# Optimization experiments

Measured on AMD Instinct MI355X. Metric: run time of the kernel, lower is better.

## Reference

```python
import jax, jax.numpy as jnp
import numpy as np

MAX_ITER = 10
EPS = 1e-4


def setup_inputs() -> dict:
    key = jax.random.key(0)
    k1, k2, k3 = jax.random.split(key, 3)
    B, N, M = 64, 1024, 1024
    s = jax.random.uniform(k1, (B, N, M), dtype=jnp.float32)
    nrows = jax.random.randint(k2, (B,), 0, N, dtype=jnp.int64 if jax.config.read('jax_enable_x64') else jnp.int32)
    ncols = jax.random.randint(k3, (B,), 0, M, dtype=nrows.dtype)
    return {"s": s, "nrows": nrows, "ncols": ncols}


def _sinkhorn(s, nrows, ncols):
    # Faithful to torch Sinkhorn.forward with exp=False, dummy_row=False.
    # The torch code builds [B,N,N]/[B,M,M] block-of-ones matrices and matmuls;
    # mathematically this is a masked column-sum (even iters) / row-sum (odd iters)
    # over the valid nrows[b] x ncols[b] block, followed by division inside the
    # block and zeroing outside it.
    B, N, M = s.shape
    row_mask = jnp.arange(N)[None, :] < nrows[:, None]            # [B, N]
    col_mask = jnp.arange(M)[None, :] < ncols[:, None]            # [B, M]
    mask = row_mask[:, :, None] & col_mask[:, None, :]            # [B, N, M]

    out = s + EPS
    for i in range(MAX_ITER):
        if i % 2 == 0:
            # column sums over valid rows -> [B, 1, M]
            sm = jnp.sum(jnp.where(row_mask[:, :, None], out, 0.0), axis=1, keepdims=True)
        else:
            # row sums over valid cols -> [B, N, 1]
            sm = jnp.sum(jnp.where(col_mask[:, None, :], out, 0.0), axis=2, keepdims=True)
        sm = jnp.where(sm == 0, 1.0, sm)  # guard (only affects masked-out entries)
        out = jnp.where(mask, out / sm, 0.0)
    return out


def reference(s, nrows, ncols):
    return _sinkhorn(s, nrows, ncols)
```

## Files before the change

kernel.cpp:

```cpp
#include <hip/hip_runtime.h>
#include <hip/hip_fp16.h>

#define EPS 1e-4f
constexpr int N_DIM  = 1024;
constexpr int M_DIM  = 1024;
constexpr int BATCH  = 64;
constexpr int NB     = 1024;
constexpr int NXCD   = 8;
constexpr int SLOTS  = NB / NXCD;
constexpr int NPHASE = 5;
constexpr int WPAD   = 256;
constexpr int CH     = 16;
constexpr int Q8MIN  = 64;


typedef float v4f __attribute__((ext_vector_type(4)));
__device__ __forceinline__ float4 ntload4(const float* p) {
    v4f v = __builtin_nontemporal_load((const v4f*)p);
    return make_float4(v[0], v[1], v[2], v[3]);
}
__device__ __forceinline__ void ntstore4(float* p, float4 q) {
    v4f v = {q.x, q.y, q.z, q.w};
    __builtin_nontemporal_store(v, (v4f*)p);
}

__device__ __forceinline__ unsigned enc8(float v) {
    int u = (int)__float_as_uint(v) + 0x00040000 - 0x3C000000;
    int b = u >> 19;
    return (unsigned)min(max(b, 16), 127);
}
__device__ __forceinline__ float dec8(unsigned b) {
    return b ? __uint_as_float((b << 19) + 0x3C000000u) : 0.f;
}

__global__ void zero_cnt(unsigned int* cnt) {
    const int t = threadIdx.x;
    if (t < NPHASE * BATCH) cnt[t] = 0u;
}

__device__ __forceinline__ void bat_barrier(unsigned int* cnt, int idx,
                                            unsigned int nact) {
    __syncthreads();
    if (threadIdx.x == 0) {
        __threadfence();
        atomicAdd(&cnt[idx], 1u);
        while (__hip_atomic_load(&cnt[idx], __ATOMIC_ACQUIRE,
                                 __HIP_MEMORY_SCOPE_AGENT) < nact)
            __builtin_amdgcn_s_sleep(8);
    }
    __syncthreads();
    __threadfence();
}

__device__ __forceinline__ void tp_store(__half* tp, size_t idx, float4 v) {
    union { __half2 h2[2]; uint2 u; } pk;
    pk.h2[0] = __floats2half2_rn(v.x, v.y);
    pk.h2[1] = __floats2half2_rn(v.z, v.w);
    *(uint2*)(tp + idx) = pk.u;
}

__global__ __launch_bounds__(256, 4)
void sinkhorn_xcd(const float* __restrict__ s,
                  const int* __restrict__ nrows,
                  const int* __restrict__ ncols,
                  __half* __restrict__ h,
                  __half* __restrict__ tp0,
                  __half* __restrict__ tp1,
                  unsigned int* __restrict__ cnt,
                  float* __restrict__ out)
{
    const int tid = threadIdx.x, lane = tid & 63, wv = tid >> 6;
    __shared__ int sR[BATCH];
    __shared__ int sBx[BATCH];
    __shared__ int sNb[BATCH];
    __shared__ int sSt[BATCH];

    if (tid < BATCH) sR[tid] = nrows[tid];
    __syncthreads();
    if (tid == 0) {
        int load[NXCD]; int W[NXCD]; int Cn[NXCD]; int acc[NXCD];
        for (int x = 0; x < NXCD; ++x) { load[x] = 0; W[x] = 0; Cn[x] = 0; acc[x] = 0; }
        for (int i = 0; i < BATCH; ++i) {
            const int w = sR[i] + WPAD;
            int best = 0;
            for (int x = 1; x < NXCD; ++x) if (load[x] < load[best]) best = x;
            sBx[i] = best; load[best] += w;
        }
        for (int i = 0; i < BATCH; ++i) { W[sBx[i]] += sR[i] + WPAD; Cn[sBx[i]]++; }
        for (int i = 0; i < BATCH; ++i) {
            const int x = sBx[i];
            int nb = 1 + (int)(((long)(SLOTS - Cn[x]) * (sR[i] + WPAD)) / W[x]);
            sNb[i] = nb; sSt[i] = acc[x]; acc[x] += nb;
        }
        sR[0] = sR[0];
    }
    __syncthreads();

    const int g    = blockIdx.x;
    const int xcd  = g & (NXCD - 1);
    const int slot = g >> 3;
    int b = -1, l = 0;
    for (int i = 0; i < BATCH; ++i) {
        if (sBx[i] == xcd && slot >= sSt[i] && slot < sSt[i] + sNb[i]) {
            b = i; l = slot - sSt[i]; break;
        }
    }
    if (b < 0) return;

    const int nbb = sNb[b];
    const int R = sR[b], C = ncols[b];
    const size_t base = (size_t)b * N_DIM * M_DIM;
    const float4 z4 = make_float4(0.f, 0.f, 0.f, 0.f);

    for (int n = R + l; n < N_DIM; n += nbb)
        ntstore4(out + base + (size_t)n * M_DIM + tid * 4, z4);
    if (R == 0) return;

    const int CR = (R + nbb - 1) / nbb;
    const unsigned int nact = (unsigned int)((R + CR - 1) / CR);
    if ((unsigned int)l >= nact) return;
    const int n0 = l * CR;
    const int rows = min(R - n0, CR);
    const bool hi = (C > 512);
    const bool q8 = (R >= Q8MIN && C >= Q8MIN);
    unsigned char* __restrict__ h8 = (unsigned char*)(h + base);

    const int tbase0 = xcd * SLOTS + sSt[b];

    __shared__ float clds[M_DIM];
    __shared__ float tp_lds[4][M_DIM];

    {
        const int m = tid * 4;
        float4 acc = z4;
        if (m < C) {
            for (int nn = 0; nn < rows; ++nn) {
                const size_t roff = (size_t)(n0 + nn) * M_DIM + m;
                float4 v = ntload4(s + base + roff);
                v.x += EPS;
                v.y = (m + 1 < C) ? v.y + EPS : 0.f;
                v.z = (m + 2 < C) ? v.z + EPS : 0.f;
                v.w = (m + 3 < C) ? v.w + EPS : 0.f;
                acc.x += v.x; acc.y += v.y; acc.z += v.z; acc.w += v.w;
                if (q8) {
                    unsigned b0 = enc8(v.x);
                    unsigned b1 = (v.y > 0.f) ? enc8(v.y) : 0u;
                    unsigned b2 = (v.z > 0.f) ? enc8(v.z) : 0u;
                    unsigned b3 = (v.w > 0.f) ? enc8(v.w) : 0u;
                    *(unsigned*)(h8 + roff) = b0 | (b1 << 8) | (b2 << 16) | (b3 << 24);
                } else {
                    union { __half2 h2[2]; uint2 u2; } pk;
                    pk.h2[0] = __floats2half2_rn(v.x, v.y);
                    pk.h2[1] = __floats2half2_rn(v.z, v.w);
                    *(uint2*)(h + base + roff) = pk.u2;
                }
            }
        } else if (m < 512 || hi) {
            for (int nn = 0; nn < rows; ++nn) {
                const size_t roff = (size_t)(n0 + nn) * M_DIM + m;
                if (q8) *(unsigned*)(h8 + roff) = 0u;
                else    *(uint2*)(h + base + roff) = make_uint2(0u, 0u);
            }
        }
        if (m < 512 || hi)
            tp_store(tp0, (size_t)(tbase0 + l) * M_DIM + m, acc);
    }
    bat_barrier(cnt, 0 * BATCH + b, nact);

    const __half* tpIn  = tp0;
    __half*       tpOut = tp1;
    float crlo[8], crhi[8];

    for (int step = 0; step < 4; ++step) {
        {
            const int m = tid * 4;
            if (m < 512 || hi) {
                float4 sum = z4;
                for (unsigned int cc = 0; cc < nact; ++cc) {
                    uint2 raw = *(const uint2*)(tpIn + (size_t)(tbase0 + cc) * M_DIM + m);
                    const __half2* hp = (const __half2*)&raw;
                    float2 f0 = __half22float2(hp[0]);
                    float2 f1 = __half22float2(hp[1]);
                    sum.x += f0.x; sum.y += f0.y; sum.z += f1.x; sum.w += f1.y;
                }
                float4 cv;
                cv.x = (sum.x == 0.f) ? 1.f : 1.f / sum.x;
                cv.y = (sum.y == 0.f) ? 1.f : 1.f / sum.y;
                cv.z = (sum.z == 0.f) ? 1.f : 1.f / sum.z;
                cv.w = (sum.w == 0.f) ? 1.f : 1.f / sum.w;
                *(float4*)&clds[m] = cv;
            }
        }
        __syncthreads();
        {
            float4 a  = *(const float4*)&clds[lane * 8];
            float4 bb = *(const float4*)&clds[lane * 8 + 4];
            crlo[0]=a.x; crlo[1]=a.y; crlo[2]=a.z; crlo[3]=a.w;
            crlo[4]=bb.x; crlo[5]=bb.y; crlo[6]=bb.z; crlo[7]=bb.w;
            if (hi) {
                float4 d = *(const float4*)&clds[512 + lane * 8];
                float4 e = *(const float4*)&clds[512 + lane * 8 + 4];
                crhi[0]=d.x; crhi[1]=d.y; crhi[2]=d.z; crhi[3]=d.w;
                crhi[4]=e.x; crhi[5]=e.y; crhi[6]=e.z; crhi[7]=e.w;
            }
        }

        float tplo[8] = {0,0,0,0,0,0,0,0};
        float tphi[8] = {0,0,0,0,0,0,0,0};

        for (int nn = wv; nn < rows; nn += 4) {
            float flo[8], fhi[8];
            if (q8) {
                const unsigned char* hrow = h8 + (size_t)(n0 + nn) * M_DIM;
                uint2 rlo = *(const uint2*)(hrow + lane * 8);
#pragma unroll
                for (int k = 0; k < 4; ++k) flo[k]     = dec8((rlo.x >> (8*k)) & 0xffu);
#pragma unroll
                for (int k = 0; k < 4; ++k) flo[4 + k] = dec8((rlo.y >> (8*k)) & 0xffu);
                if (hi) {
                    uint2 rhi = *(const uint2*)(hrow + 512 + lane * 8);
#pragma unroll
                    for (int k = 0; k < 4; ++k) fhi[k]     = dec8((rhi.x >> (8*k)) & 0xffu);
#pragma unroll
                    for (int k = 0; k < 4; ++k) fhi[4 + k] = dec8((rhi.y >> (8*k)) & 0xffu);
                }
            } else {
                const __half* hrow = h + base + (size_t)(n0 + nn) * M_DIM;
                uint4 rlo = *(const uint4*)(hrow + lane * 8);
                const __half2* hp = (const __half2*)&rlo;
#pragma unroll
                for (int k = 0; k < 4; ++k) {
                    float2 f = __half22float2(hp[k]);
                    flo[2*k] = f.x; flo[2*k+1] = f.y;
                }
                if (hi) {
                    uint4 rhi = *(const uint4*)(hrow + 512 + lane * 8);
                    const __half2* hq = (const __half2*)&rhi;
#pragma unroll
                    for (int k = 0; k < 4; ++k) {
                        float2 f = __half22float2(hq[k]);
                        fhi[2*k] = f.x; fhi[2*k+1] = f.y;
                    }
                }
            }
            float dot = 0.f;
#pragma unroll
            for (int k = 0; k < 8; ++k) dot += flo[k] * crlo[k];
            if (hi) {
#pragma unroll
                for (int k = 0; k < 8; ++k) dot += fhi[k] * crhi[k];
            }
#pragma unroll
            for (int off = 32; off; off >>= 1) dot += __shfl_xor(dot, off);
            const float r = (dot == 0.f) ? 1.f : 1.f / dot;
#pragma unroll
            for (int k = 0; k < 8; ++k) tplo[k] += flo[k] * r;
            if (hi) {
#pragma unroll
                for (int k = 0; k < 8; ++k) tphi[k] += fhi[k] * r;
            }
        }

#pragma unroll
        for (int k = 0; k < 8; ++k) tp_lds[wv][lane * 8 + k] = tplo[k];
        if (hi) {
#pragma unroll
            for (int k = 0; k < 8; ++k) tp_lds[wv][512 + lane * 8 + k] = tphi[k];
        }
        __syncthreads();
        {
            const int m = tid * 4;
            if (m < 512 || hi) {
                float4 s0 = *(const float4*)&tp_lds[0][m];
                float4 s1 = *(const float4*)&tp_lds[1][m];
                float4 s2 = *(const float4*)&tp_lds[2][m];
                float4 s3 = *(const float4*)&tp_lds[3][m];
                tp_store(tpOut, (size_t)(tbase0 + l) * M_DIM + m,
                         make_float4(s0.x+s1.x+s2.x+s3.x, s0.y+s1.y+s2.y+s3.y,
                                     s0.z+s1.z+s2.z+s3.z, s0.w+s1.w+s2.w+s3.w));
            }
        }
        bat_barrier(cnt, (1 + step) * BATCH + b, nact);
        const __half* ti = tpOut; tpOut = (__half*)tpIn; tpIn = ti;
    }

    {
        const int m = tid * 4;
        if (m < 512 || hi) {
            float4 sum = z4;
            for (unsigned int cc = 0; cc < nact; ++cc) {
                uint2 raw = *(const uint2*)(tpIn + (size_t)(tbase0 + cc) * M_DIM + m);
                const __half2* hp = (const __half2*)&raw;
                float2 f0 = __half22float2(hp[0]);
                float2 f1 = __half22float2(hp[1]);
                sum.x += f0.x; sum.y += f0.y; sum.z += f1.x; sum.w += f1.y;
            }
            float4 cv;
            cv.x = (sum.x == 0.f) ? 1.f : 1.f / sum.x;
            cv.y = (sum.y == 0.f) ? 1.f : 1.f / sum.y;
            cv.z = (sum.z == 0.f) ? 1.f : 1.f / sum.z;
            cv.w = (sum.w == 0.f) ? 1.f : 1.f / sum.w;
            *(float4*)&clds[m] = cv;
        }
    }
    __syncthreads();
    {
        float4 a  = *(const float4*)&clds[lane * 8];
        float4 bb = *(const float4*)&clds[lane * 8 + 4];
        crlo[0]=a.x; crlo[1]=a.y; crlo[2]=a.z; crlo[3]=a.w;
        crlo[4]=bb.x; crlo[5]=bb.y; crlo[6]=bb.z; crlo[7]=bb.w;
        if (hi) {
            float4 d = *(const float4*)&clds[512 + lane * 8];
            float4 e = *(const float4*)&clds[512 + lane * 8 + 4];
            crhi[0]=d.x; crhi[1]=d.y; crhi[2]=d.z; crhi[3]=d.w;
            crhi[4]=e.x; crhi[5]=e.y; crhi[6]=e.z; crhi[7]=e.w;
        }
    }
    for (int nn = wv; nn < rows; nn += 4) {
        const int n = n0 + nn;
        float* orow = out + base + (size_t)n * M_DIM;
        float flo[8], fhi[8];
        if (q8) {
            const unsigned char* hrow = h8 + (size_t)n * M_DIM;
            uint2 rlo = *(const uint2*)(hrow + lane * 8);
#pragma unroll
            for (int k = 0; k < 4; ++k) flo[k]     = dec8((rlo.x >> (8*k)) & 0xffu);
#pragma unroll
            for (int k = 0; k < 4; ++k) flo[4 + k] = dec8((rlo.y >> (8*k)) & 0xffu);
            if (hi) {
                uint2 rhi = *(const uint2*)(hrow + 512 + lane * 8);
#pragma unroll
                for (int k = 0; k < 4; ++k) fhi[k]     = dec8((rhi.x >> (8*k)) & 0xffu);
#pragma unroll
                for (int k = 0; k < 4; ++k) fhi[4 + k] = dec8((rhi.y >> (8*k)) & 0xffu);
            }
        } else {
            const __half* hrow = h + base + (size_t)n * M_DIM;
            uint4 rlo = *(const uint4*)(hrow + lane * 8);
            const __half2* hp = (const __half2*)&rlo;
#pragma unroll
            for (int k = 0; k < 4; ++k) {
                float2 f = __half22float2(hp[k]);
                flo[2*k] = f.x; flo[2*k+1] = f.y;
            }
            if (hi) {
                uint4 rhi = *(const uint4*)(hrow + 512 + lane * 8);
                const __half2* hq = (const __half2*)&rhi;
#pragma unroll
                for (int k = 0; k < 4; ++k) {
                    float2 f = __half22float2(hq[k]);
                    fhi[2*k] = f.x; fhi[2*k+1] = f.y;
                }
            }
        }
        float dot = 0.f;
#pragma unroll
        for (int k = 0; k < 8; ++k) dot += flo[k] * crlo[k];
        if (hi) {
#pragma unroll
            for (int k = 0; k < 8; ++k) dot += fhi[k] * crhi[k];
        }
#pragma unroll
        for (int off = 32; off; off >>= 1) dot += __shfl_xor(dot, off);
        const float r = (dot == 0.f) ? 1.f : 1.f / dot;

        ntstore4(orow + lane * 8,     make_float4(flo[0]*r*crlo[0], flo[1]*r*crlo[1],
                                                  flo[2]*r*crlo[2], flo[3]*r*crlo[3]));
        ntstore4(orow + lane * 8 + 4, make_float4(flo[4]*r*crlo[4], flo[5]*r*crlo[5],
                                                  flo[6]*r*crlo[6], flo[7]*r*crlo[7]));
        float4 o2 = z4, o3 = z4;
        if (hi) {
            o2 = make_float4(fhi[0]*r*crhi[0], fhi[1]*r*crhi[1],
                             fhi[2]*r*crhi[2], fhi[3]*r*crhi[3]);
            o3 = make_float4(fhi[4]*r*crhi[4], fhi[5]*r*crhi[5],
                             fhi[6]*r*crhi[6], fhi[7]*r*crhi[7]);
        }
        ntstore4(orow + 512 + lane * 8,     o2);
        ntstore4(orow + 512 + lane * 8 + 4, o3);
    }
}

constexpr int FCROWS = N_DIM / CH;

__global__ __launch_bounds__(256)
void conv_col0(const float* __restrict__ s, const int* __restrict__ nrows,
               const int* __restrict__ ncols, __half* __restrict__ h,
               float* __restrict__ tp0) {
    const int b  = blockIdx.y;
    const int mt = blockIdx.x & 3;
    const int ch = blockIdx.x >> 2;
    const int R = nrows[b], C = ncols[b];
    const int n0 = ch * FCROWS;
    if (n0 >= R) return;
    const int lane = threadIdx.x & 63, wv = threadIdx.x >> 6;
    const int m = mt * 256 + lane * 4;
    const int nend = min(R, n0 + FCROWS);
    const size_t base = (size_t)b * N_DIM * M_DIM;

    float4 acc = make_float4(0.f, 0.f, 0.f, 0.f);
    if (mt * 256 < C) {
        for (int n = n0 + wv; n < nend; n += 4) {
            float4 v = *(const float4*)(s + base + (size_t)n * M_DIM + m);
            v.x = (m + 0 < C) ? v.x + EPS : 0.f;
            v.y = (m + 1 < C) ? v.y + EPS : 0.f;
            v.z = (m + 2 < C) ? v.z + EPS : 0.f;
            v.w = (m + 3 < C) ? v.w + EPS : 0.f;
            acc.x += v.x; acc.y += v.y; acc.z += v.z; acc.w += v.w;
            union { __half2 h2[2]; uint2 u2; } pk;
            pk.h2[0] = __floats2half2_rn(v.x, v.y);
            pk.h2[1] = __floats2half2_rn(v.z, v.w);
            *(uint2*)(h + base + (size_t)n * M_DIM + m) = pk.u2;
        }
    } else {
        const uint2 z = make_uint2(0u, 0u);
        for (int n = n0 + wv; n < nend; n += 4)
            *(uint2*)(h + base + (size_t)n * M_DIM + m) = z;
    }
    __shared__ float4 red[4][64];
    red[wv][lane] = acc;
    __syncthreads();
    if (wv == 0) {
        float4 a0 = red[0][lane], a1 = red[1][lane],
               a2 = red[2][lane], a3 = red[3][lane];
        *(float4*)(tp0 + (size_t)(ch * BATCH + b) * M_DIM + m) =
            make_float4(a0.x+a1.x+a2.x+a3.x, a0.y+a1.y+a2.y+a3.y,
                        a0.z+a1.z+a2.z+a3.z, a0.w+a1.w+a2.w+a3.w);
    }
}

template <bool FINAL>
__global__ __launch_bounds__(256)
void row_step(const __half* __restrict__ h, const int* __restrict__ nrows,
              const int* __restrict__ ncols, const float* __restrict__ tpIn,
              float* __restrict__ tpOut, float* __restrict__ out) {
    const int b  = blockIdx.y;
    const int ch = blockIdx.x;
    const int R = nrows[b], C = ncols[b];
    const int n0 = ch * FCROWS;
    if (!FINAL && n0 >= R) return;
    const int lane = threadIdx.x & 63, wv = threadIdx.x >> 6;
    const size_t base = (size_t)b * N_DIM * M_DIM;
    const bool hi = (C > 512);
    const bool anyrows = (n0 < R);

    __shared__ float clds[M_DIM];
    __shared__ float tp_lds[4][M_DIM];

    float crlo[8], crhi[8];
    if (anyrows) {
        const int nch = min(CH, (R + FCROWS - 1) / FCROWS);
        const int t4 = threadIdx.x * 4;
        if (hi || t4 < 512) {
            float4 sum = make_float4(0.f, 0.f, 0.f, 0.f);
            for (int cc = 0; cc < nch; ++cc) {
                float4 p = *(const float4*)(tpIn + (size_t)(cc * BATCH + b) * M_DIM + t4);
                sum.x += p.x; sum.y += p.y; sum.z += p.z; sum.w += p.w;
            }
            float4 cv;
            cv.x = (sum.x == 0.f) ? 1.f : 1.f / sum.x;
            cv.y = (sum.y == 0.f) ? 1.f : 1.f / sum.y;
            cv.z = (sum.z == 0.f) ? 1.f : 1.f / sum.z;
            cv.w = (sum.w == 0.f) ? 1.f : 1.f / sum.w;
            *(float4*)&clds[t4] = cv;
        }
        __syncthreads();
        float4 a = *(const float4*)&clds[lane * 8];
        float4 bb = *(const float4*)&clds[lane * 8 + 4];
        crlo[0]=a.x; crlo[1]=a.y; crlo[2]=a.z; crlo[3]=a.w;
        crlo[4]=bb.x; crlo[5]=bb.y; crlo[6]=bb.z; crlo[7]=bb.w;
        if (hi) {
            float4 d = *(const float4*)&clds[512 + lane * 8];
            float4 e = *(const float4*)&clds[512 + lane * 8 + 4];
            crhi[0]=d.x; crhi[1]=d.y; crhi[2]=d.z; crhi[3]=d.w;
            crhi[4]=e.x; crhi[5]=e.y; crhi[6]=e.z; crhi[7]=e.w;
        }
    }

    float tplo[8] = {0,0,0,0,0,0,0,0};
    float tphi[8] = {0,0,0,0,0,0,0,0};

    for (int i = 0; i < 16; ++i) {
        const int n = n0 + wv * 16 + i;
        if (n < R) {
            const __half* hrow = h + base + (size_t)n * M_DIM;
            uint4 rlo = *(const uint4*)(hrow + lane * 8);
            float flo[8], fhi[8];
            const __half2* hp = (const __half2*)&rlo;
#pragma unroll
            for (int k = 0; k < 4; ++k) {
                float2 f = __half22float2(hp[k]);
                flo[2*k] = f.x; flo[2*k+1] = f.y;
            }
            float dot = 0.f;
#pragma unroll
            for (int k = 0; k < 8; ++k) dot += flo[k] * crlo[k];
            if (hi) {
                uint4 rhi = *(const uint4*)(hrow + 512 + lane * 8);
                const __half2* hq = (const __half2*)&rhi;
#pragma unroll
                for (int k = 0; k < 4; ++k) {
                    float2 f = __half22float2(hq[k]);
                    fhi[2*k] = f.x; fhi[2*k+1] = f.y;
                }
#pragma unroll
                for (int k = 0; k < 8; ++k) dot += fhi[k] * crhi[k];
            }
#pragma unroll
            for (int off = 32; off; off >>= 1) dot += __shfl_xor(dot, off);
            const float r = (dot == 0.f) ? 1.f : 1.f / dot;

            if (FINAL) {
                float* orow = out + base + (size_t)n * M_DIM;
                *(float4*)(orow + lane * 8)     = make_float4(flo[0]*r*crlo[0], flo[1]*r*crlo[1],
                                                              flo[2]*r*crlo[2], flo[3]*r*crlo[3]);
                *(float4*)(orow + lane * 8 + 4) = make_float4(flo[4]*r*crlo[4], flo[5]*r*crlo[5],
                                                              flo[6]*r*crlo[6], flo[7]*r*crlo[7]);
                float4 o2 = make_float4(0.f,0.f,0.f,0.f), o3 = o2;
                if (hi) {
                    o2 = make_float4(fhi[0]*r*crhi[0], fhi[1]*r*crhi[1],
                                     fhi[2]*r*crhi[2], fhi[3]*r*crhi[3]);
                    o3 = make_float4(fhi[4]*r*crhi[4], fhi[5]*r*crhi[5],
                                     fhi[6]*r*crhi[6], fhi[7]*r*crhi[7]);
                }
                *(float4*)(orow + 512 + lane * 8)     = o2;
                *(float4*)(orow + 512 + lane * 8 + 4) = o3;
            } else {
#pragma unroll
                for (int k = 0; k < 8; ++k) tplo[k] += flo[k] * r;
                if (hi) {
#pragma unroll
                    for (int k = 0; k < 8; ++k) tphi[k] += fhi[k] * r;
                }
            }
        } else if (FINAL) {
            float* orow = out + base + (size_t)n * M_DIM;
            const float4 z = make_float4(0.f, 0.f, 0.f, 0.f);
            *(float4*)(orow + lane * 8)           = z;
            *(float4*)(orow + lane * 8 + 4)       = z;
            *(float4*)(orow + 512 + lane * 8)     = z;
            *(float4*)(orow + 512 + lane * 8 + 4) = z;
        }
    }

    if (!FINAL) {
#pragma unroll
        for (int k = 0; k < 8; ++k) tp_lds[wv][lane * 8 + k] = tplo[k];
        if (hi) {
#pragma unroll
            for (int k = 0; k < 8; ++k) tp_lds[wv][512 + lane * 8 + k] = tphi[k];
        }
        __syncthreads();
        const int t4 = threadIdx.x * 4;
        if (hi || t4 < 512) {
            float4 s0 = *(const float4*)&tp_lds[0][t4];
            float4 s1 = *(const float4*)&tp_lds[1][t4];
            float4 s2 = *(const float4*)&tp_lds[2][t4];
            float4 s3 = *(const float4*)&tp_lds[3][t4];
            *(float4*)(tpOut + (size_t)(ch * BATCH + b) * M_DIM + t4) =
                make_float4(s0.x+s1.x+s2.x+s3.x, s0.y+s1.y+s2.y+s3.y,
                            s0.z+s1.z+s2.z+s3.z, s0.w+s1.w+s2.w+s3.w);
        }
    }
}

extern "C" void kernel_launch(void* const* d_in, const int* in_sizes, int n_in,
                              void* d_out, int out_size, void* d_ws, size_t ws_size,
                              hipStream_t stream) {
    const float* s     = (const float*)d_in[0];
    const int*   nrows = (const int*)d_in[1];
    const int*   ncols = (const int*)d_in[2];
    float*       out   = (float*)d_out;

    const size_t hElems   = (size_t)BATCH * N_DIM * M_DIM;
    const size_t tpRegion = (size_t)16 * 1024 * 1024;
    const size_t need     = hElems * 2 + tpRegion + NPHASE * BATCH * 4;

    if (ws_size >= need) {
        __half* h    = (__half*)d_ws;
        char*   tpRg = (char*)(h + hElems);
        unsigned int* cnt = (unsigned int*)(tpRg + tpRegion);

        int dev = 0, numCU = 0, perCU = 0;
        hipGetDevice(&dev);
        hipDeviceGetAttribute(&numCU, hipDeviceAttributeMultiprocessorCount, dev);
        hipOccupancyMaxActiveBlocksPerMultiprocessor(&perCU, sinkhorn_xcd, 256, 0);

        if ((long long)perCU * numCU >= NB) {
            __half* tp0 = (__half*)tpRg;
            __half* tp1 = tp0 + (size_t)NB * M_DIM;
            zero_cnt<<<1, 320, 0, stream>>>(cnt);
            void* args[] = {(void*)&s, (void*)&nrows, (void*)&ncols, (void*)&h,
                            (void*)&tp0, (void*)&tp1, (void*)&cnt, (void*)&out};
            hipLaunchCooperativeKernel((void*)sinkhorn_xcd, dim3(NB),
                                       dim3(256), args, 0, stream);
            return;
        }

        float* tp0f = (float*)tpRg;
        float* tp1f = tp0f + (size_t)CH * BATCH * M_DIM;
        dim3 convGrid(4 * CH, BATCH), kGrid(CH, BATCH);
        conv_col0<<<convGrid, 256, 0, stream>>>(s, nrows, ncols, h, tp0f);
        row_step<false><<<kGrid, 256, 0, stream>>>(h, nrows, ncols, tp0f, tp1f, out);
        row_step<false><<<kGrid, 256, 0, stream>>>(h, nrows, ncols, tp1f, tp0f, out);
        row_step<false><<<kGrid, 256, 0, stream>>>(h, nrows, ncols, tp0f, tp1f, out);
        row_step<false><<<kGrid, 256, 0, stream>>>(h, nrows, ncols, tp1f, tp0f, out);
        row_step<true ><<<kGrid, 256, 0, stream>>>(h, nrows, ncols, tp0f, tp1f, out);
        return;
    }
}
```

Measured before the change: 204.8 us.

## Keep compressed matrix rows in registers instead of global scratch buffer

The persistent cooperative kernel now keeps each block's quantized rows (8-bit or packed half) in per-thread registers, up to 48 rows per block. This removes the global write and the repeated global re-reads of the compressed copy on every Sinkhorn step. Rows beyond that cap are re-read from the fp32 input each step. The block scheduler also guarantees enough blocks per batch so most rows fit in registers. The register arrays may raise VGPR pressure, which could drop occupancy below the 4 blocks per CU the cooperative launch needs and force the multi-kernel fallback path.

Result: no change. 206.8 us (+1.0%).

```diff
diff --git a/kernel.cpp b/kernel.cpp
--- a/kernel.cpp
+++ b/kernel.cpp
@@ -10,8 +10,9 @@
 constexpr int SLOTS  = NB / NXCD;
 constexpr int NPHASE = 5;
 constexpr int WPAD   = 256;
+constexpr int RCAP   = 48;
+constexpr int NSLOT  = RCAP / 4;
 constexpr int CH     = 16;
-constexpr int Q8MIN  = 64;
 
 
 typedef float v4f __attribute__((ext_vector_type(4)));
@@ -31,6 +32,23 @@
 }
 __device__ __forceinline__ float dec8(unsigned b) {
     return b ? __uint_as_float((b << 19) + 0x3C000000u) : 0.f;
+}
+__device__ __forceinline__ unsigned pk8(float a, float b, float c, float d) {
+    unsigned b0 = (a > 0.f) ? enc8(a) : 0u;
+    unsigned b1 = (b > 0.f) ? enc8(b) : 0u;
+    unsigned b2 = (c > 0.f) ? enc8(c) : 0u;
+    unsigned b3 = (d > 0.f) ? enc8(d) : 0u;
+    return b0 | (b1 << 8) | (b2 << 16) | (b3 << 24);
+}
+__device__ __forceinline__ unsigned pkh(float a, float b) {
+    union { __half2 h; unsigned u; } pk;
+    pk.h = __floats2half2_rn(a, b);
+    return pk.u;
+}
+__device__ __forceinline__ void uph(unsigned u, float* f) {
+    union { unsigned uu; __half2 h; } pk; pk.uu = u;
+    float2 r = __half22float2(pk.h);
+    f[0] = r.x; f[1] = r.y;
 }
 
 __global__ void zero_cnt(unsigned int* cnt) {
@@ -59,40 +77,71 @@
     *(uint2*)(tp + idx) = pk.u;
 }
 
+__device__ __forceinline__ void load_srow(const float* srow, int lane, int C,
+                                          bool hi, float* v, float* w) {
+    float4 a0 = ntload4(srow + lane * 8);
+    float4 a1 = ntload4(srow + lane * 8 + 4);
+    const int c0 = lane * 8;
+    v[0] = (c0 + 0 < C) ? a0.x + EPS : 0.f;
+    v[1] = (c0 + 1 < C) ? a0.y + EPS : 0.f;
+    v[2] = (c0 + 2 < C) ? a0.z + EPS : 0.f;
+    v[3] = (c0 + 3 < C) ? a0.w + EPS : 0.f;
+    v[4] = (c0 + 4 < C) ? a1.x + EPS : 0.f;
+    v[5] = (c0 + 5 < C) ? a1.y + EPS : 0.f;
+    v[6] = (c0 + 6 < C) ? a1.z + EPS : 0.f;
+    v[7] = (c0 + 7 < C) ? a1.w + EPS : 0.f;
+    if (hi) {
+        float4 b0 = ntload4(srow + 512 + lane * 8);
+        float4 b1 = ntload4(srow + 512 + lane * 8 + 4);
+        const int c1 = 512 + lane * 8;
+        w[0] = (c1 + 0 < C) ? b0.x + EPS : 0.f;
+        w[1] = (c1 + 1 < C) ? b0.y + EPS : 0.f;
+        w[2] = (c1 + 2 < C) ? b0.z + EPS : 0.f;
+        w[3] = (c1 + 3 < C) ? b0.w + EPS : 0.f;
+        w[4] = (c1 + 4 < C) ? b1.x + EPS : 0.f;
+        w[5] = (c1 + 5 < C) ? b1.y + EPS : 0.f;
+        w[6] = (c1 + 6 < C) ? b1.z + EPS : 0.f;
+        w[7] = (c1 + 7 < C) ? b1.w + EPS : 0.f;
+    }
+}
+
 __global__ __launch_bounds__(256, 4)
-void sinkhorn_xcd(const float* __restrict__ s,
+void sinkhorn_reg(const float* __restrict__ s,
                   const int* __restrict__ nrows,
                   const int* __restrict__ ncols,
-                  __half* __restrict__ h,
                   __half* __restrict__ tp0,
                   __half* __restrict__ tp1,
                   unsigned int* __restrict__ cnt,
                   float* __restrict__ out)
 {
     const int tid = threadIdx.x, lane = tid & 63, wv = tid >> 6;
-    __shared__ int sR[BATCH];
-    __shared__ int sBx[BATCH];
-    __shared__ int sNb[BATCH];
-    __shared__ int sSt[BATCH];
+    __shared__ int sR[BATCH], sBx[BATCH], sNb[BATCH], sSt[BATCH];
 
     if (tid < BATCH) sR[tid] = nrows[tid];
     __syncthreads();
     if (tid == 0) {
-        int load[NXCD]; int W[NXCD]; int Cn[NXCD]; int acc[NXCD];
-        for (int x = 0; x < NXCD; ++x) { load[x] = 0; W[x] = 0; Cn[x] = 0; acc[x] = 0; }
+        int load[NXCD], W[NXCD], Mn[NXCD], acc[NXCD];
+        for (int x = 0; x < NXCD; ++x) { load[x] = W[x] = Mn[x] = acc[x] = 0; }
         for (int i = 0; i < BATCH; ++i) {
             const int w = sR[i] + WPAD;
             int best = 0;
             for (int x = 1; x < NXCD; ++x) if (load[x] < load[best]) best = x;
             sBx[i] = best; load[best] += w;
         }
-        for (int i = 0; i < BATCH; ++i) { W[sBx[i]] += sR[i] + WPAD; Cn[sBx[i]]++; }
         for (int i = 0; i < BATCH; ++i) {
             const int x = sBx[i];
-            int nb = 1 + (int)(((long)(SLOTS - Cn[x]) * (sR[i] + WPAD)) / W[x]);
+            W[x]  += sR[i] + WPAD;
+            Mn[x] += max(1, (sR[i] + RCAP - 1) / RCAP);
+        }
+        for (int i = 0; i < BATCH; ++i) {
+            const int x = sBx[i];
+            const int minb = max(1, (sR[i] + RCAP - 1) / RCAP);
+            const int rem  = SLOTS - Mn[x];
+            const int extra = (rem > 0) ? (int)(((long)rem * (sR[i] + WPAD)) / W[x]) : 0;
+            int nb = minb + extra;
+            if (acc[x] + nb > SLOTS) nb = SLOTS - acc[x];
             sNb[i] = nb; sSt[i] = acc[x]; acc[x] += nb;
         }
-        sR[0] = sR[0];
     }
     __syncthreads();
 
@@ -122,54 +171,71 @@
     const int n0 = l * CR;
     const int rows = min(R - n0, CR);
     const bool hi = (C > 512);
-    const bool q8 = (R >= Q8MIN && C >= Q8MIN);
-    unsigned char* __restrict__ h8 = (unsigned char*)(h + base);
-
     const int tbase0 = xcd * SLOTS + sSt[b];
 
     __shared__ float clds[M_DIM];
     __shared__ float tp_lds[4][M_DIM];
 
+    unsigned h0[NSLOT], h1[NSLOT], h2[NSLOT], h3[NSLOT];
+    float tplo[8] = {0,0,0,0,0,0,0,0};
+    float tphi[8] = {0,0,0,0,0,0,0,0};
+    float crlo[8], crhi[8];
+
+#pragma unroll
+    for (int i = 0; i < NSLOT; ++i) {
+        h0[i] = h1[i] = h2[i] = h3[i] = 0u;
+        const int rr = wv + 4 * i;
+        if (rr < rows) {
+            float v[8], w[8];
+            load_srow(s + base + (size_t)(n0 + rr) * M_DIM, lane, C, hi, v, w);
+#pragma unroll
+            for (int k = 0; k < 8; ++k) tplo[k] += v[k];
+            if (hi) {
+#pragma unroll
+                for (int k = 0; k < 8; ++k) tphi[k] += w[k];
+                h0[i] = pk8(v[0], v[1], v[2], v[3]);
+                h1[i] = pk8(v[4], v[5], v[6], v[7]);
+                h2[i] = pk8(w[0], w[1], w[2], w[3]);
+                h3[i] = pk8(w[4], w[5], w[6], w[7]);
+            } else {
+                h0[i] = pkh(v[0], v[1]); h1[i] = pkh(v[2], v[3]);
+                h2[i] = pkh(v[4], v[5]); h3[i] = pkh(v[6], v[7]);
+            }
+        }
+    }
+    for (int rr = RCAP + wv; rr < rows; rr += 4) {
+        float v[8], w[8];
+        load_srow(s + base + (size_t)(n0 + rr) * M_DIM, lane, C, hi, v, w);
+#pragma unroll
+        for (int k = 0; k < 8; ++k) tplo[k] += v[k];
+        if (hi) {
+#pragma unroll
+            for (int k = 0; k < 8; ++k) tphi[k] += w[k];
+        }
+    }
     {
+#pragma unroll
+        for (int k = 0; k < 8; ++k) tp_lds[wv][lane * 8 + k] = tplo[k];
+        if (hi) {
+#pragma unroll
+            for (int k = 0; k < 8; ++k) tp_lds[wv][512 + lane * 8 + k] = tphi[k];
+        }
+        __syncthreads();
         const int m = tid * 4;
-        float4 acc = z4;
-        if (m < C) {
-            for (int nn = 0; nn < rows; ++nn) {
-                const size_t roff = (size_t)(n0 + nn) * M_DIM + m;
-                float4 v = ntload4(s + base + roff);
-                v.x += EPS;
-                v.y = (m + 1 < C) ? v.y + EPS : 0.f;
-                v.z = (m + 2 < C) ? v.z + EPS : 0.f;
-                v.w = (m + 3 < C) ? v.w + EPS : 0.f;
-                acc.x += v.x; acc.y += v.y; acc.z += v.z; acc.w += v.w;
-                if (q8) {
-                    unsigned b0 = enc8(v.x);
-                    unsigned b1 = (v.y > 0.f) ? enc8(v.y) : 0u;
-                    unsigned b2 = (v.z > 0.f) ? enc8(v.z) : 0u;
-                    unsigned b3 = (v.w > 0.f) ? enc8(v.w) : 0u;
-                    *(unsigned*)(h8 + roff) = b0 | (b1 << 8) | (b2 << 16) | (b3 << 24);
-                } else {
-                    union { __half2 h2[2]; uint2 u2; } pk;
-                    pk.h2[0] = __floats2half2_rn(v.x, v.y);
-                    pk.h2[1] = __floats2half2_rn(v.z, v.w);
-                    *(uint2*)(h + base + roff) = pk.u2;
-                }
-            }
-        } else if (m < 512 || hi) {
-            for (int nn = 0; nn < rows; ++nn) {
-                const size_t roff = (size_t)(n0 + nn) * M_DIM + m;
-                if (q8) *(unsigned*)(h8 + roff) = 0u;
-                else    *(uint2*)(h + base + roff) = make_uint2(0u, 0u);
-            }
-        }
-        if (m < 512 || hi)
-            tp_store(tp0, (size_t)(tbase0 + l) * M_DIM + m, acc);
+        if (m < 512 || hi) {
+            float4 s0 = *(const float4*)&tp_lds[0][m];
+            float4 s1 = *(const float4*)&tp_lds[1][m];
+            float4 s2 = *(const float4*)&tp_lds[2][m];
+            float4 s3 = *(const float4*)&tp_lds[3][m];
+            tp_store(tp0, (size_t)(tbase0 + l) * M_DIM + m,
+                     make_float4(s0.x+s1.x+s2.x+s3.x, s0.y+s1.y+s2.y+s3.y,
+                                 s0.z+s1.z+s2.z+s3.z, s0.w+s1.w+s2.w+s3.w));
+        }
     }
     bat_barrier(cnt, 0 * BATCH + b, nact);
 
     const __half* tpIn  = tp0;
     __half*       tpOut = tp1;
-    float crlo[8], crhi[8];
 
     for (int step = 0; step < 4; ++step) {
         {
@@ -192,83 +258,82 @@
             }
         }
         __syncthreads();
-        {
-            float4 a  = *(const float4*)&clds[lane * 8];
-            float4 bb = *(const float4*)&clds[lane * 8 + 4];
-            crlo[0]=a.x; crlo[1]=a.y; crlo[2]=a.z; crlo[3]=a.w;
-            crlo[4]=bb.x; crlo[5]=bb.y; crlo[6]=bb.z; crlo[7]=bb.w;
-            if (hi) {
-                float4 d = *(const float4*)&clds[512 + lane * 8];
-                float4 e = *(const float4*)&clds[512 + lane * 8 + 4];
-                crhi[0]=d.x; crhi[1]=d.y; crhi[2]=d.z; crhi[3]=d.w;
-                crhi[4]=e.x; crhi[5]=e.y; crhi[6]=e.z; crhi[7]=e.w;
-            }
-        }
-
-        float tplo[8] = {0,0,0,0,0,0,0,0};
-        float tphi[8] = {0,0,0,0,0,0,0,0};
-
-        for (int nn = wv; nn < rows; nn += 4) {
-            float flo[8], fhi[8];
-            if (q8) {
-                const unsigned char* hrow = h8 + (size_t)(n0 + nn) * M_DIM;
-                uint2 rlo = *(const uint2*)(hrow + lane * 8);
-#pragma unroll
-                for (int k = 0; k < 4; ++k) flo[k]     = dec8((rlo.x >> (8*k)) & 0xffu);
-#pragma unroll
-                for (int k = 0; k < 4; ++k) flo[4 + k] = dec8((rlo.y >> (8*k)) & 0xffu);
+#pragma unroll
+        for (int k = 0; k < 8; ++k) crlo[k] = clds[lane * 8 + k];
+        if (hi) {
+#pragma unroll
+            for (int k = 0; k < 8; ++k) crhi[k] = clds[512 + lane * 8 + k];
+        }
+
+#pragma unroll
+        for (int k = 0; k < 8; ++k) { tplo[k] = 0.f; tphi[k] = 0.f; }
+
+#pragma unroll
+        for (int i = 0; i < NSLOT; ++i) {
+            const int rr = wv + 4 * i;
+            if (rr < rows) {
+                float flo[8], fhi[8];
                 if (hi) {
-                    uint2 rhi = *(const uint2*)(hrow + 512 + lane * 8);
-#pragma unroll
-                    for (int k = 0; k < 4; ++k) fhi[k]     = dec8((rhi.x >> (8*k)) & 0xffu);
-#pragma unroll
-                    for (int k = 0; k < 4; ++k) fhi[4 + k] = dec8((rhi.y >> (8*k)) & 0xffu);
+                    const unsigned r0 = h0[i], r1 = h1[i], r2 = h2[i], r3 = h3[i];
+                    flo[0]=dec8(r0&0xffu); flo[1]=dec8((r0>>8)&0xffu);
+                    flo[2]=dec8((r0>>16)&0xffu); flo[3]=dec8(r0>>24);
+                    flo[4]=dec8(r1&0xffu); flo[5]=dec8((r1>>8)&0xffu);
+                    flo[6]=dec8((r1>>16)&0xffu); flo[7]=dec8(r1>>24);
+                    fhi[0]=dec8(r2&0xffu); fhi[1]=dec8((r2>>8)&0xffu);
+                    fhi[2]=dec8((r2>>16)&0xffu); fhi[3]=dec8(r2>>24);
+                    fhi[4]=dec8(r3&0xffu); fhi[5]=dec8((r3>>8)&0xffu);
+                    fhi[6]=dec8((r3>>16)&0xffu); fhi[7]=dec8(r3>>24);
+                } else {
+                    uph(h0[i], &flo[0]); uph(h1[i], &flo[2]);
+                    uph(h2[i], &flo[4]); uph(h3[i], &flo[6]);
                 }
-            } else {
-                const __half* hrow = h + base + (size_t)(n0 + nn) * M_DIM;
-                uint4 rlo = *(const uint4*)(hrow + lane * 8);
-                const __half2* hp = (const __half2*)&rlo;
-#pragma unroll
-                for (int k = 0; k < 4; ++k) {
-                    float2 f = __half22float2(hp[k]);
-                    flo[2*k] = f.x; flo[2*k+1] = f.y;
+                float dot = 0.f;
+#pragma unroll
+                for (int k = 0; k < 8; ++k) dot += flo[k] * crlo[k];
+                if (hi) {
+#pragma unroll
+                    for (int k = 0; k < 8; ++k) dot += fhi[k] * crhi[k];
                 }
+#pragma unroll
+                for (int off = 32; off; off >>= 1) dot += __shfl_xor(dot, off);
+                const float r = (dot == 0.f) ? 1.f : 1.f / dot;
+#pragma unroll
+                for (int k = 0; k < 8; ++k) tplo[k] += flo[k] * r;
                 if (hi) {
-                    uint4 rhi = *(const uint4*)(hrow + 512 + lane * 8);
-                    const __half2* hq = (const __half2*)&rhi;
-#pragma unroll
-                    for (int k = 0; k < 4; ++k) {
-                        float2 f = __half22float2(hq[k]);
-                        fhi[2*k] = f.x; fhi[2*k+1] = f.y;
-                    }
+#pragma unroll
+                    for (int k = 0; k < 8; ++k) tphi[k] += fhi[k] * r;
                 }
             }
+        }
+        for (int rr = RCAP + wv; rr < rows; rr += 4) {
+            float v[8], w[8];
+            load_srow(s + base + (size_t)(n0 + rr) * M_DIM, lane, C, hi, v, w);
             float dot = 0.f;
 #pragma unroll
-            for (int k = 0; k < 8; ++k) dot += flo[k] * crlo[k];
-            if (hi) {
-#pragma unroll
-                for (int k = 0; k < 8; ++k) dot += fhi[k] * crhi[k];
+            for (int k = 0; k < 8; ++k) dot += v[k] * crlo[k];
+            if (hi) {
+#pragma unroll
+                for (int k = 0; k < 8; ++k) dot += w[k] * crhi[k];
             }
 #pragma unroll
             for (int off = 32; off; off >>= 1) dot += __shfl_xor(dot, off);
             const float r = (dot == 0.f) ? 1.f : 1.f / dot;
 #pragma unroll
-            for (int k = 0; k < 8; ++k) tplo[k] += flo[k] * r;
-            if (hi) {
-#pragma unroll
-                for (int k = 0; k < 8; ++k) tphi[k] += fhi[k] * r;
-            }
-        }
-
-#pragma unroll
-        for (int k = 0; k < 8; ++k) tp_lds[wv][lane * 8 + k] = tplo[k];
-        if (hi) {
-#pragma unroll
-            for (int k = 0; k < 8; ++k) tp_lds[wv][512 + lane * 8 + k] = tphi[k];
-        }
-        __syncthreads();
+            for (int k = 0; k < 8; ++k) tplo[k] += v[k] * r;
+            if (hi) {
+#pragma unroll
+                for (int k = 0; k < 8; ++k) tphi[k] += w[k] * r;
+            }
+        }
+
         {
+#pragma unroll
+            for (int k = 0; k < 8; ++k) tp_lds[wv][lane * 8 + k] = tplo[k];
+            if (hi) {
+#pragma unroll
+                for (int k = 0; k < 8; ++k) tp_lds[wv][512 + lane * 8 + k] = tphi[k];
+            }
+            __syncthreads();
             const int m = tid * 4;
             if (m < 512 || hi) {
                 float4 s0 = *(const float4*)&tp_lds[0][m];
@@ -304,76 +369,83 @@
         }
     }
     __syncthreads();
-    {
-        float4 a  = *(const float4*)&clds[lane * 8];
-        float4 bb = *(const float4*)&clds[lane * 8 + 4];
-        crlo[0]=a.x; crlo[1]=a.y; crlo[2]=a.z; crlo[3]=a.w;
-        crlo[4]=bb.x; crlo[5]=bb.y; crlo[6]=bb.z; crlo[7]=bb.w;
+#pragma unroll
+    for (int k = 0; k < 8; ++k) crlo[k] = clds[lane * 8 + k];
+    if (hi) {
+#pragma unroll
+        for (int k = 0; k < 8; ++k) crhi[k] = clds[512 + lane * 8 + k];
+    }
+
+#pragma unroll
+    for (int i = 0; i < NSLOT; ++i) {
+        const int rr = wv + 4 * i;
+        if (rr < rows) {
+            float flo[8], fhi[8];
+            if (hi) {
+                const unsigned r0 = h0[i], r1 = h1[i], r2 = h2[i], r3 = h3[i];
+                flo[0]=dec8(r0&0xffu); flo[1]=dec8((r0>>8)&0xffu);
+                flo[2]=dec8((r0>>16)&0xffu); flo[3]=dec8(r0>>24);
+                flo[4]=dec8(r1&0xffu); flo[5]=dec8((r1>>8)&0xffu);
+                flo[6]=dec8((r1>>16)&0xffu); flo[7]=dec8(r1>>24);
+                fhi[0]=dec8(r2&0xffu); fhi[1]=dec8((r2>>8)&0xffu);
+                fhi[2]=dec8((r2>>16)&0xffu); fhi[3]=dec8(r2>>24);
+                fhi[4]=dec8(r3&0xffu); fhi[5]=dec8((r3>>8)&0xffu);
+                fhi[6]=dec8((r3>>16)&0xffu); fhi[7]=dec8(r3>>24);
+            } else {
+                uph(h0[i], &flo[0]); uph(h1[i], &flo[2]);
+                uph(h2[i], &flo[4]); uph(h3[i], &flo[6]);
+            }
+            float dot = 0.f;
+#pragma unroll
+            for (int k = 0; k < 8; ++k) dot += flo[k] * crlo[k];
+            if (hi) {
+#pragma unroll
+                for (int k = 0; k < 8; ++k) dot += fhi[k] * crhi[k];
+            }
+#pragma unroll
+            for (int off = 32; off; off >>= 1) dot += __shfl_xor(dot, off);
+            const float r = (dot == 0.f) ? 1.f : 1.f / dot;
+
+            float* orow = out + base + (size_t)(n0 + rr) * M_DIM;
+            ntstore4(orow + lane * 8,     make_float4(flo[0]*r*crlo[0], flo[1]*r*crlo[1],
+                                                      flo[2]*r*crlo[2], flo[3]*r*crlo[3]));
+            ntstore4(orow + lane * 8 + 4, make_float4(flo[4]*r*crlo[4], flo[5]*r*crlo[5],
+                                                      flo[6]*r*crlo[6], flo[7]*r*crlo[7]));
+            float4 o2 = z4, o3 = z4;
+            if (hi) {
+                o2 = make_float4(fhi[0]*r*crhi[0], fhi[1]*r*crhi[1],
+                                 fhi[2]*r*crhi[2], fhi[3]*r*crhi[3]);
+                o3 = make_float4(fhi[4]*r*crhi[4], fhi[5]*r*crhi[5],
+                                 fhi[6]*r*crhi[6], fhi[7]*r*crhi[7]);
+            }
+            ntstore4(orow + 512 + lane * 8,     o2);
+            ntstore4(orow + 512 + lane * 8 + 4, o3);
+        }
+    }
+    for (int rr = RCAP + wv; rr < rows; rr += 4) {
+        float v[8], w[8];
+        load_srow(s + base + (size_t)(n0 + rr) * M_DIM, lane, C, hi, v, w);
+        float dot = 0.f;
+#pragma unroll
+        for (int k = 0; k < 8; ++k) dot += v[k] * crlo[k];
         if (hi) {
-            float4 d = *(const float4*)&clds[512 + lane * 8];
-            float4 e = *(const float4*)&clds[512 + lane * 8 + 4];
-            crhi[0]=d.x; crhi[1]=d.y; crhi[2]=d.z; crhi[3]=d.w;
-            crhi[4]=e.x; crhi[5]=e.y; crhi[6]=e.z; crhi[7]=e.w;
-        }
-    }
-    for (int nn = wv; nn < rows; nn += 4) {
-        const int n = n0 + nn;
-        float* orow = out + base + (size_t)n * M_DIM;
-        float flo[8], fhi[8];
-        if (q8) {
-            const unsigned char* hrow = h8 + (size_t)n * M_DIM;
-            uint2 rlo = *(const uint2*)(hrow + lane * 8);
-#pragma unroll
-            for (int k = 0; k < 4; ++k) flo[k]     = dec8((rlo.x >> (8*k)) & 0xffu);
-#pragma unroll
-            for (int k = 0; k < 4; ++k) flo[4 + k] = dec8((rlo.y >> (8*k)) & 0xffu);
-            if (hi) {
-                uint2 rhi = *(const uint2*)(hrow + 512 + lane * 8);
-#pragma unroll
-                for (int k = 0; k < 4; ++k) fhi[k]     = dec8((rhi.x >> (8*k)) & 0xffu);
-#pragma unroll
-                for (int k = 0; k < 4; ++k) fhi[4 + k] = dec8((rhi.y >> (8*k)) & 0xffu);
-            }
-        } else {
-            const __half* hrow = h + base + (size_t)n * M_DIM;
-            uint4 rlo = *(const uint4*)(hrow + lane * 8);
-            const __half2* hp = (const __half2*)&rlo;
-#pragma unroll
-            for (int k = 0; k < 4; ++k) {
-                float2 f = __half22float2(hp[k]);
-                flo[2*k] = f.x; flo[2*k+1] = f.y;
-            }
-            if (hi) {
-                uint4 rhi = *(const uint4*)(hrow + 512 + lane * 8);
-                const __half2* hq = (const __half2*)&rhi;
-#pragma unroll
-                for (int k = 0; k < 4; ++k) {
-                    float2 f = __half22float2(hq[k]);
-                    fhi[2*k] = f.x; fhi[2*k+1] = f.y;
-                }
-            }
-        }
-        float dot = 0.f;
-#pragma unroll
-        for (int k = 0; k < 8; ++k) dot += flo[k] * crlo[k];
-        if (hi) {
-#pragma unroll
-            for (int k = 0; k < 8; ++k) dot += fhi[k] * crhi[k];
+#pragma unroll
+            for (int k = 0; k < 8; ++k) dot += w[k] * crhi[k];
         }
 #pragma unroll
         for (int off = 32; off; off >>= 1) dot += __shfl_xor(dot, off);
         const float r = (dot == 0.f) ? 1.f : 1.f / dot;
-
-        ntstore4(orow + lane * 8,     make_float4(flo[0]*r*crlo[0], flo[1]*r*crlo[1],
-                                                  flo[2]*r*crlo[2], flo[3]*r*crlo[3]));
-        ntstore4(orow + lane * 8 + 4, make_float4(flo[4]*r*crlo[4], flo[5]*r*crlo[5],
-                                                  flo[6]*r*crlo[6], flo[7]*r*crlo[7]));
+        float* orow = out + base + (size_t)(n0 + rr) * M_DIM;
+        ntstore4(orow + lane * 8,     make_float4(v[0]*r*crlo[0], v[1]*r*crlo[1],
+                                                  v[2]*r*crlo[2], v[3]*r*crlo[3]));
+        ntstore4(orow + lane * 8 + 4, make_float4(v[4]*r*crlo[4], v[5]*r*crlo[5],
+                                                  v[6]*r*crlo[6], v[7]*r*crlo[7]));
         float4 o2 = z4, o3 = z4;
         if (hi) {
-            o2 = make_float4(fhi[0]*r*crhi[0], fhi[1]*r*crhi[1],
-                             fhi[2]*r*crhi[2], fhi[3]*r*crhi[3]);
-            o3 = make_float4(fhi[4]*r*crhi[4], fhi[5]*r*crhi[5],
-                             fhi[6]*r*crhi[6], fhi[7]*r*crhi[7]);
+            o2 = make_float4(w[0]*r*crhi[0], w[1]*r*crhi[1],
+                             w[2]*r*crhi[2], w[3]*r*crhi[3]);
+            o3 = make_float4(w[4]*r*crhi[4], w[5]*r*crhi[5],
+                             w[6]*r*crhi[6], w[7]*r*crhi[7]);
         }
         ntstore4(orow + 512 + lane * 8,     o2);
         ntstore4(orow + 512 + lane * 8 + 4, o3);
@@ -583,15 +655,15 @@
         int dev = 0, numCU = 0, perCU = 0;
         hipGetDevice(&dev);
         hipDeviceGetAttribute(&numCU, hipDeviceAttributeMultiprocessorCount, dev);
-        hipOccupancyMaxActiveBlocksPerMultiprocessor(&perCU, sinkhorn_xcd, 256, 0);
+        hipOccupancyMaxActiveBlocksPerMultiprocessor(&perCU, sinkhorn_reg, 256, 0);
 
         if ((long long)perCU * numCU >= NB) {
             __half* tp0 = (__half*)tpRg;
             __half* tp1 = tp0 + (size_t)NB * M_DIM;
             zero_cnt<<<1, 320, 0, stream>>>(cnt);
-            void* args[] = {(void*)&s, (void*)&nrows, (void*)&ncols, (void*)&h,
+            void* args[] = {(void*)&s, (void*)&nrows, (void*)&ncols,
                             (void*)&tp0, (void*)&tp1, (void*)&cnt, (void*)&out};
-            hipLaunchCooperativeKernel((void*)sinkhorn_xcd, dim3(NB),
+            hipLaunchCooperativeKernel((void*)sinkhorn_reg, dim3(NB),
                                        dim3(256), args, 0, stream);
             return;
         }
```
